# Kernel tuning notes

Hardware: AMD Instinct MI355X
Metric: run time of the kernel (lower is better)

The kernel has to match this reference:

```python
import jax, jax.numpy as jnp
import numpy as np

EPS = 1.0
MAX_ITER = 5
THRESH = 0.01
P_EXP = 2


def setup_inputs() -> dict:
    key = jax.random.key(0)
    k1, k2 = jax.random.split(key)
    x = jax.random.normal(k1, (2, 4096, 3), dtype=jnp.float32)
    y = jax.random.normal(k2, (2, 4096, 3), dtype=jnp.float32)
    return {"x": x, "y": y}


def _cost_matrix(x, y, p=P_EXP):
    # |x_i - y_j|^p summed over feature dim -> (B, P1, P2)
    return jnp.sum(jnp.abs(x[:, :, None, :] - y[:, None, :, :]) ** p, axis=-1)


def reference(x, y):
    C = _cost_matrix(x, y)  # (B, P1, P2)
    B, P1, P2 = C.shape
    log_mu = jnp.full((B, P1), jnp.log(1.0 / P1), dtype=C.dtype)
    log_nu = jnp.full((B, P2), jnp.log(1.0 / P2), dtype=C.dtype)

    def M(u, v):
        # (-C_ij + u_i + v_j) / eps
        return (-C + u[:, :, None] + v[:, None, :]) / EPS

    u = jnp.zeros((B, P1), dtype=C.dtype)
    v = jnp.zeros((B, P2), dtype=C.dtype)
    err = jnp.array(jnp.inf, dtype=C.dtype)
    done = jnp.zeros((), dtype=bool)

    # Unrolled fixed-count loop; `done` freezes updates to emulate the
    # data-dependent early break in the original torch code.
    for i in range(MAX_ITER):
        if i % 2 == 0:
            u_new = EPS * (log_mu - jax.nn.logsumexp(M(u, v), axis=-1)) + u
            err_new = jnp.mean(jnp.sum(jnp.abs(u_new - u), axis=-1))
            u = jnp.where(done, u, u_new)
            err = jnp.where(done, err, err_new)
        else:
            v_new = EPS * (log_nu - jax.nn.logsumexp(M(u, v), axis=-2)) + v
            v = jnp.where(done, v, v_new)
        done = done | (err < THRESH)

    pi = jnp.exp(M(u, v))  # transport plan (B, P1, P2)
    approx_corr_1 = jnp.argmax(pi, axis=-1)  # (B, P1)
    approx_corr_2 = jnp.argmax(pi, axis=-2)  # (B, P2)
    # u.shape[0] == v.shape[0] (== B) so torch takes the sum(dim=-2).sum()
    # branch; both branches reduce to a full sum.
    distance = jnp.sum(pi * C)
    return distance, approx_corr_1, approx_corr_2
```

## Files before the change

kernel.cpp:

```cpp
#include <hip/hip_runtime.h>
#include <math.h>

#define P 4096
#define NB 2
#define NROWS (NB * P)
#define THREADS 512
#define NWAVE (THREADS / 64)
#define R 8
#define NCHUNK (P / THREADS)
#define NBLK (NROWS / R)
#define LOG_INV_P (-8.317766166719343f)
#define INV_P (0.000244140625f)
#define ERR_T (0.02f)

#define WS_U   0
#define WS_V   NROWS
#define WS_ERR (2 * NROWS)
#define WS_SOA 16640


__global__ void prep_kernel(const float* __restrict__ x, const float* __restrict__ y,
                            float* __restrict__ ws, float* __restrict__ out) {
    const int idx = blockIdx.x * blockDim.x + threadIdx.x;
    float* __restrict__ soa = ws + WS_SOA;
    if (idx < NROWS) {
        soa[0 * NROWS + idx] = x[idx * 3 + 0];
        soa[1 * NROWS + idx] = x[idx * 3 + 1];
        soa[2 * NROWS + idx] = x[idx * 3 + 2];
        ws[WS_V + idx] = 0.0f;
    } else {
        const int k = idx - NROWS;
        soa[3 * NROWS + k] = y[k * 3 + 0];
        soa[4 * NROWS + k] = y[k * 3 + 1];
        soa[5 * NROWS + k] = y[k * 3 + 2];
    }
    if (idx < 4) ws[WS_ERR + idx] = 0.0f;
    if (idx == 4) out[0] = 0.0f;
}

template <int WITH_ERR, int ZERO_W>
__global__ __launch_bounds__(THREADS, 4) void lse_single(
    const float* __restrict__ rs0, const float* __restrict__ rs1,
    const float* __restrict__ rs2,
    const float* __restrict__ cs0, const float* __restrict__ cs1,
    const float* __restrict__ cs2,
    const float* __restrict__ w,
    float* __restrict__ pot,
    float* __restrict__ err_acc,
    const float* __restrict__ chk0, const float* __restrict__ chk1)
{
    bool frozen = false;
    if (chk0) frozen = frozen || (*chk0 < ERR_T);
    if (chk1) frozen = frozen || (*chk1 < ERR_T);
    if (frozen) return;

    __shared__ float red[NWAVE * R];

    const int row0 = blockIdx.x * R;
    const int bofs = (row0 >> 12) << 12;
    const int t = threadIdx.x;
    const int wid = t >> 6, lane = t & 63;

    float xr0[R], xr1[R], xr2[R];
#pragma unroll
    for (int r = 0; r < R; r++) {
        xr0[r] = rs0[row0 + r];
        xr1[r] = rs1[row0 + r];
        xr2[r] = rs2[row0 + r];
    }
    float s[R];
#pragma unroll
    for (int r = 0; r < R; r++) s[r] = 0.0f;

#pragma unroll
    for (int k = 0; k < NCHUNK; k++) {
        const int j = bofs + t + k * THREADS;
        const float y0 = cs0[j], y1 = cs1[j], y2 = cs2[j];
        const float wj = ZERO_W ? 0.0f : w[j];
#pragma unroll
        for (int r = 0; r < R; r++) {
            const float d0 = xr0[r] - y0, d1 = xr1[r] - y1, d2 = xr2[r] - y2;
            const float c = d0 * d0 + d1 * d1 + d2 * d2;
            s[r] += __expf(wj - c);
        }
    }
#pragma unroll
    for (int r = 0; r < R; r++) {
        float v2 = s[r];
#pragma unroll
        for (int off = 32; off >= 1; off >>= 1)
            v2 += __shfl_down(v2, off, 64);
        if (lane == 0) red[wid * R + r] = v2;
    }
    __syncthreads();
    if (t < R) {
        float ssum = red[t];
#pragma unroll
        for (int w2 = 1; w2 < NWAVE; w2++) ssum += red[w2 * R + t];
        const float pn = LOG_INV_P - __logf(ssum);
        float d = 0.0f;
        if (WITH_ERR) d = fabsf(pn - (ZERO_W ? 0.0f : pot[row0 + t]));
        pot[row0 + t] = pn;
        if (WITH_ERR) {
#pragma unroll
            for (int off = R / 2; off >= 1; off >>= 1)
                d += __shfl_down(d, off, R);
            if (t == 0) atomicAdd(err_acc, d);
        }
    }
}

__global__ __launch_bounds__(THREADS, 4) void row_final(
    const float* __restrict__ rs0, const float* __restrict__ rs1,
    const float* __restrict__ rs2,
    const float* __restrict__ cs0, const float* __restrict__ cs1,
    const float* __restrict__ cs2,
    const float* __restrict__ v,
    float* __restrict__ u_out,
    float* __restrict__ corr1,
    float* __restrict__ dist)
{
    __shared__ float redS[NWAVE * R];
    __shared__ float redD[NWAVE * R];
    __shared__ float redv[NWAVE * R];
    __shared__ int   redj[NWAVE * R];

    const int row0 = blockIdx.x * R;
    const int bofs = (row0 >> 12) << 12;
    const int t = threadIdx.x;
    const int wid = t >> 6, lane = t & 63;

    float xr0[R], xr1[R], xr2[R];
#pragma unroll
    for (int r = 0; r < R; r++) {
        xr0[r] = rs0[row0 + r];
        xr1[r] = rs1[row0 + r];
        xr2[r] = rs2[row0 + r];
    }
    float S[R], D[R], bv[R];
    int bj[R];
#pragma unroll
    for (int r = 0; r < R; r++) { S[r] = 0.0f; D[r] = 0.0f; bv[r] = -INFINITY; bj[r] = 0; }

#pragma unroll
    for (int k = 0; k < NCHUNK; k++) {
        const int jj = t + k * THREADS;
        const int j = bofs + jj;
        const float y0 = cs0[j], y1 = cs1[j], y2 = cs2[j];
        const float wj = v[j];
#pragma unroll
        for (int r = 0; r < R; r++) {
            const float d0 = xr0[r] - y0, d1 = xr1[r] - y1, d2 = xr2[r] - y2;
            const float c = d0 * d0 + d1 * d1 + d2 * d2;
            const float m = wj - c;
            const float e = __expf(m);
            S[r] += e;
            D[r] += e * c;
            const bool pgt = m > bv[r];
            bj[r] = pgt ? jj : bj[r];
            bv[r] = pgt ? m : bv[r];
        }
    }
#pragma unroll
    for (int r = 0; r < R; r++) {
        float sS = S[r], sD = D[r], v2 = bv[r];
        int j2 = bj[r];
#pragma unroll
        for (int off = 32; off >= 1; off >>= 1) {
            sS += __shfl_down(sS, off, 64);
            sD += __shfl_down(sD, off, 64);
            const float ov = __shfl_down(v2, off, 64);
            const int   oj = __shfl_down(j2, off, 64);
            const bool take = (ov > v2) || (ov == v2 && oj < j2);
            v2 = take ? ov : v2;
            j2 = take ? oj : j2;
        }
        if (lane == 0) {
            redS[wid * R + r] = sS;
            redD[wid * R + r] = sD;
            redv[wid * R + r] = v2;
            redj[wid * R + r] = j2;
        }
    }
    __syncthreads();
    if (t < R) {
        float sS = redS[t], sD = redD[t], v2 = redv[t];
        int j2 = redj[t];
#pragma unroll
        for (int w2 = 1; w2 < NWAVE; w2++) {
            sS += redS[w2 * R + t];
            sD += redD[w2 * R + t];
            const float ov = redv[w2 * R + t];
            const int   oj = redj[w2 * R + t];
            const bool take = (ov > v2) || (ov == v2 && oj < j2);
            v2 = take ? ov : v2;
            j2 = take ? oj : j2;
        }
        u_out[row0 + t] = LOG_INV_P - __logf(sS);
        corr1[row0 + t] = (float)j2;
        float dp = INV_P * sD / sS;
#pragma unroll
        for (int off = R / 2; off >= 1; off >>= 1)
            dp += __shfl_down(dp, off, R);
        if (t == 0) atomicAdd(dist, dp);
    }
}

__global__ __launch_bounds__(THREADS, 4) void col_final(
    const float* __restrict__ rs0, const float* __restrict__ rs1,
    const float* __restrict__ rs2,
    const float* __restrict__ cs0, const float* __restrict__ cs1,
    const float* __restrict__ cs2,
    const float* __restrict__ u,
    float* __restrict__ corr2)
{
    __shared__ float redv[NWAVE * R];
    __shared__ int   redj[NWAVE * R];

    const int row0 = blockIdx.x * R;
    const int bofs = (row0 >> 12) << 12;
    const int t = threadIdx.x;
    const int wid = t >> 6, lane = t & 63;

    float xr0[R], xr1[R], xr2[R];
#pragma unroll
    for (int r = 0; r < R; r++) {
        xr0[r] = rs0[row0 + r];
        xr1[r] = rs1[row0 + r];
        xr2[r] = rs2[row0 + r];
    }
    float bv[R];
    int bj[R];
#pragma unroll
    for (int r = 0; r < R; r++) { bv[r] = -INFINITY; bj[r] = 0; }

#pragma unroll
    for (int k = 0; k < NCHUNK; k++) {
        const int jj = t + k * THREADS;
        const int j = bofs + jj;
        const float y0 = cs0[j], y1 = cs1[j], y2 = cs2[j];
        const float wj = u[j];
#pragma unroll
        for (int r = 0; r < R; r++) {
            const float d0 = xr0[r] - y0, d1 = xr1[r] - y1, d2 = xr2[r] - y2;
            const float c = d0 * d0 + d1 * d1 + d2 * d2;
            const float m = wj - c;
            const bool pgt = m > bv[r];
            bj[r] = pgt ? jj : bj[r];
            bv[r] = pgt ? m : bv[r];
        }
    }
#pragma unroll
    for (int r = 0; r < R; r++) {
        float v2 = bv[r];
        int j2 = bj[r];
#pragma unroll
        for (int off = 32; off >= 1; off >>= 1) {
            const float ov = __shfl_down(v2, off, 64);
            const int   oj = __shfl_down(j2, off, 64);
            const bool take = (ov > v2) || (ov == v2 && oj < j2);
            v2 = take ? ov : v2;
            j2 = take ? oj : j2;
        }
        if (lane == 0) { redv[wid * R + r] = v2; redj[wid * R + r] = j2; }
    }
    __syncthreads();
    if (t < R) {
        float v2 = redv[t];
        int j2 = redj[t];
#pragma unroll
        for (int w2 = 1; w2 < NWAVE; w2++) {
            const float ov = redv[w2 * R + t];
            const int   oj = redj[w2 * R + t];
            const bool take = (ov > v2) || (ov == v2 && oj < j2);
            v2 = take ? ov : v2;
            j2 = take ? oj : j2;
        }
        corr2[row0 + t] = (float)j2;
    }
}

extern "C" void kernel_launch(void* const* d_in, const int* in_sizes, int n_in,
                              void* d_out, int out_size, void* d_ws, size_t ws_size,
                              hipStream_t stream) {
    const float* x = (const float*)d_in[0];
    const float* y = (const float*)d_in[1];
    float* out = (float*)d_out;
    float* ws = (float*)d_ws;

    float* u = ws + WS_U;
    float* v = ws + WS_V;
    float* err = ws + WS_ERR;
    float* xs0 = ws + WS_SOA + 0 * NROWS;
    float* xs1 = ws + WS_SOA + 1 * NROWS;
    float* xs2 = ws + WS_SOA + 2 * NROWS;
    float* ys0 = ws + WS_SOA + 3 * NROWS;
    float* ys1 = ws + WS_SOA + 4 * NROWS;
    float* ys2 = ws + WS_SOA + 5 * NROWS;

    prep_kernel<<<32, 512, 0, stream>>>(x, y, ws, out);

    dim3 grid(NBLK), blk(THREADS);
    lse_single<1, 1><<<grid, blk, 0, stream>>>(xs0, xs1, xs2, ys0, ys1, ys2,
                                               v, u, &err[0], nullptr, nullptr);
    lse_single<0, 0><<<grid, blk, 0, stream>>>(ys0, ys1, ys2, xs0, xs1, xs2,
                                               u, v, nullptr, &err[0], nullptr);
    lse_single<1, 0><<<grid, blk, 0, stream>>>(xs0, xs1, xs2, ys0, ys1, ys2,
                                               v, u, &err[1], &err[0], nullptr);
    lse_single<0, 0><<<grid, blk, 0, stream>>>(ys0, ys1, ys2, xs0, xs1, xs2,
                                               u, v, nullptr, &err[0], &err[1]);
    row_final<<<grid, blk, 0, stream>>>(xs0, xs1, xs2, ys0, ys1, ys2,
                                        v, u, out + 1, out);
    col_final<<<grid, blk, 0, stream>>>(ys0, ys1, ys2, xs0, xs1, xs2,
                                        u, out + 1 + NROWS);
}
```

Measured before the change: 182.2 us.

## Expand squared distance into dot product and work in base-2 log domain

The inputs are prescaled by sqrt(log2 e), and squared norms are precomputed in the prep kernel. The column side stores doubled coordinates, so each cost term becomes three FMAs plus a norm offset fed straight into the hardware v_exp_f32 instruction. All potentials, thresholds and the distance constant are moved into the log2 domain to stay consistent. Column data for all chunks is loaded into registers up front. This cuts per-element ALU work in the compute-bound inner loops, at the cost of some cancellation error from the norm expansion and higher register use.

After: 168.9 us. 7.3% less time.

```diff
diff --git a/kernel.cpp b/kernel.cpp
--- a/kernel.cpp
+++ b/kernel.cpp
@@ -9,30 +9,45 @@
 #define R 8
 #define NCHUNK (P / THREADS)
 #define NBLK (NROWS / R)
-#define LOG_INV_P (-8.317766166719343f)
-#define INV_P (0.000244140625f)
-#define ERR_T (0.02f)
+#define SQRT_LOG2E 1.2011224087864498f
+#define LOG2_INV_P (-12.0f)
+#define ERR_T2 0.028853900817779268f
+#define C_DIST 1.6922538540598323e-4f
 
 #define WS_U   0
 #define WS_V   NROWS
 #define WS_ERR (2 * NROWS)
 #define WS_SOA 16640
 
+
+__device__ __forceinline__ float exp2_hw(float x) {
+    float r;
+    asm("v_exp_f32 %0, %1" : "=v"(r) : "v"(x));
+    return r;
+}
 
 __global__ void prep_kernel(const float* __restrict__ x, const float* __restrict__ y,
                             float* __restrict__ ws, float* __restrict__ out) {
     const int idx = blockIdx.x * blockDim.x + threadIdx.x;
     float* __restrict__ soa = ws + WS_SOA;
     if (idx < NROWS) {
-        soa[0 * NROWS + idx] = x[idx * 3 + 0];
-        soa[1 * NROWS + idx] = x[idx * 3 + 1];
-        soa[2 * NROWS + idx] = x[idx * 3 + 2];
+        const float a0 = x[idx * 3 + 0] * SQRT_LOG2E;
+        const float a1 = x[idx * 3 + 1] * SQRT_LOG2E;
+        const float a2 = x[idx * 3 + 2] * SQRT_LOG2E;
+        soa[0 * NROWS + idx] = a0;
+        soa[1 * NROWS + idx] = a1;
+        soa[2 * NROWS + idx] = a2;
+        soa[3 * NROWS + idx] = a0 * a0 + a1 * a1 + a2 * a2;
         ws[WS_V + idx] = 0.0f;
     } else {
         const int k = idx - NROWS;
-        soa[3 * NROWS + k] = y[k * 3 + 0];
-        soa[4 * NROWS + k] = y[k * 3 + 1];
-        soa[5 * NROWS + k] = y[k * 3 + 2];
+        const float a0 = y[k * 3 + 0] * SQRT_LOG2E;
+        const float a1 = y[k * 3 + 1] * SQRT_LOG2E;
+        const float a2 = y[k * 3 + 2] * SQRT_LOG2E;
+        soa[4 * NROWS + k] = a0 + a0;
+        soa[5 * NROWS + k] = a1 + a1;
+        soa[6 * NROWS + k] = a2 + a2;
+        soa[7 * NROWS + k] = a0 * a0 + a1 * a1 + a2 * a2;
     }
     if (idx < 4) ws[WS_ERR + idx] = 0.0f;
     if (idx == 4) out[0] = 0.0f;
@@ -40,18 +55,18 @@
 
 template <int WITH_ERR, int ZERO_W>
 __global__ __launch_bounds__(THREADS, 4) void lse_single(
-    const float* __restrict__ rs0, const float* __restrict__ rs1,
-    const float* __restrict__ rs2,
-    const float* __restrict__ cs0, const float* __restrict__ cs1,
-    const float* __restrict__ cs2,
-    const float* __restrict__ w,
-    float* __restrict__ pot,
+    const float* __restrict__ rc0, const float* __restrict__ rc1,
+    const float* __restrict__ rc2, const float* __restrict__ rn,
+    const float* __restrict__ cc0, const float* __restrict__ cc1,
+    const float* __restrict__ cc2, const float* __restrict__ cn,
+    const float* __restrict__ w2,
+    float* __restrict__ pot2,
     float* __restrict__ err_acc,
     const float* __restrict__ chk0, const float* __restrict__ chk1)
 {
     bool frozen = false;
-    if (chk0) frozen = frozen || (*chk0 < ERR_T);
-    if (chk1) frozen = frozen || (*chk1 < ERR_T);
+    if (chk0) frozen = frozen || (*chk0 < ERR_T2);
+    if (chk1) frozen = frozen || (*chk1 < ERR_T2);
     if (frozen) return;
 
     __shared__ float red[NWAVE * R];
@@ -60,28 +75,37 @@
     const int bofs = (row0 >> 12) << 12;
     const int t = threadIdx.x;
     const int wid = t >> 6, lane = t & 63;
-
-    float xr0[R], xr1[R], xr2[R];
-#pragma unroll
-    for (int r = 0; r < R; r++) {
-        xr0[r] = rs0[row0 + r];
-        xr1[r] = rs1[row0 + r];
-        xr2[r] = rs2[row0 + r];
-    }
+    const int jbase = bofs + t;
+
+    float r0[R], r1[R], r2[R], rnm[R];
+#pragma unroll
+    for (int r = 0; r < R; r++) {
+        r0[r] = rc0[row0 + r];
+        r1[r] = rc1[row0 + r];
+        r2[r] = rc2[row0 + r];
+        rnm[r] = rn[row0 + r];
+    }
+    float c0[NCHUNK], c1[NCHUNK], c2[NCHUNK], a[NCHUNK];
+#pragma unroll
+    for (int k = 0; k < NCHUNK; k++) {
+        const int j = jbase + k * THREADS;
+        c0[k] = cc0[j];
+        c1[k] = cc1[j];
+        c2[k] = cc2[j];
+        a[k] = (ZERO_W ? 0.0f : w2[j]) - cn[j];
+    }
+
     float s[R];
 #pragma unroll
     for (int r = 0; r < R; r++) s[r] = 0.0f;
 
 #pragma unroll
     for (int k = 0; k < NCHUNK; k++) {
-        const int j = bofs + t + k * THREADS;
-        const float y0 = cs0[j], y1 = cs1[j], y2 = cs2[j];
-        const float wj = ZERO_W ? 0.0f : w[j];
 #pragma unroll
         for (int r = 0; r < R; r++) {
-            const float d0 = xr0[r] - y0, d1 = xr1[r] - y1, d2 = xr2[r] - y2;
-            const float c = d0 * d0 + d1 * d1 + d2 * d2;
-            s[r] += __expf(wj - c);
+            const float b = a[k] - rnm[r];
+            const float m2 = fmaf(c0[k], r0[r], fmaf(c1[k], r1[r], fmaf(c2[k], r2[r], b)));
+            s[r] += exp2_hw(m2);
         }
     }
 #pragma unroll
@@ -96,11 +120,11 @@
     if (t < R) {
         float ssum = red[t];
 #pragma unroll
-        for (int w2 = 1; w2 < NWAVE; w2++) ssum += red[w2 * R + t];
-        const float pn = LOG_INV_P - __logf(ssum);
+        for (int w = 1; w < NWAVE; w++) ssum += red[w * R + t];
+        const float pn = LOG2_INV_P - __log2f(ssum);
         float d = 0.0f;
-        if (WITH_ERR) d = fabsf(pn - (ZERO_W ? 0.0f : pot[row0 + t]));
-        pot[row0 + t] = pn;
+        if (WITH_ERR) d = fabsf(pn - (ZERO_W ? 0.0f : pot2[row0 + t]));
+        pot2[row0 + t] = pn;
         if (WITH_ERR) {
 #pragma unroll
             for (int off = R / 2; off >= 1; off >>= 1)
@@ -111,12 +135,12 @@
 }
 
 __global__ __launch_bounds__(THREADS, 4) void row_final(
-    const float* __restrict__ rs0, const float* __restrict__ rs1,
-    const float* __restrict__ rs2,
-    const float* __restrict__ cs0, const float* __restrict__ cs1,
-    const float* __restrict__ cs2,
-    const float* __restrict__ v,
-    float* __restrict__ u_out,
+    const float* __restrict__ rc0, const float* __restrict__ rc1,
+    const float* __restrict__ rc2, const float* __restrict__ rn,
+    const float* __restrict__ cc0, const float* __restrict__ cc1,
+    const float* __restrict__ cc2, const float* __restrict__ cn,
+    const float* __restrict__ w2,
+    float* __restrict__ u2_out,
     float* __restrict__ corr1,
     float* __restrict__ dist)
 {
@@ -129,14 +153,27 @@
     const int bofs = (row0 >> 12) << 12;
     const int t = threadIdx.x;
     const int wid = t >> 6, lane = t & 63;
-
-    float xr0[R], xr1[R], xr2[R];
-#pragma unroll
-    for (int r = 0; r < R; r++) {
-        xr0[r] = rs0[row0 + r];
-        xr1[r] = rs1[row0 + r];
-        xr2[r] = rs2[row0 + r];
-    }
+    const int jbase = bofs + t;
+
+    float r0[R], r1[R], r2[R], rnm[R];
+#pragma unroll
+    for (int r = 0; r < R; r++) {
+        r0[r] = rc0[row0 + r];
+        r1[r] = rc1[row0 + r];
+        r2[r] = rc2[row0 + r];
+        rnm[r] = rn[row0 + r];
+    }
+    float c0[NCHUNK], c1[NCHUNK], c2[NCHUNK], a[NCHUNK], wv[NCHUNK];
+#pragma unroll
+    for (int k = 0; k < NCHUNK; k++) {
+        const int j = jbase + k * THREADS;
+        c0[k] = cc0[j];
+        c1[k] = cc1[j];
+        c2[k] = cc2[j];
+        wv[k] = w2[j];
+        a[k] = wv[k] - cn[j];
+    }
+
     float S[R], D[R], bv[R];
     int bj[R];
 #pragma unroll
@@ -144,21 +181,16 @@
 
 #pragma unroll
     for (int k = 0; k < NCHUNK; k++) {
-        const int jj = t + k * THREADS;
-        const int j = bofs + jj;
-        const float y0 = cs0[j], y1 = cs1[j], y2 = cs2[j];
-        const float wj = v[j];
 #pragma unroll
         for (int r = 0; r < R; r++) {
-            const float d0 = xr0[r] - y0, d1 = xr1[r] - y1, d2 = xr2[r] - y2;
-            const float c = d0 * d0 + d1 * d1 + d2 * d2;
-            const float m = wj - c;
-            const float e = __expf(m);
+            const float b = a[k] - rnm[r];
+            const float m2 = fmaf(c0[k], r0[r], fmaf(c1[k], r1[r], fmaf(c2[k], r2[r], b)));
+            const float e = exp2_hw(m2);
             S[r] += e;
-            D[r] += e * c;
-            const bool pgt = m > bv[r];
-            bj[r] = pgt ? jj : bj[r];
-            bv[r] = pgt ? m : bv[r];
+            D[r] = fmaf(e, wv[k] - m2, D[r]);
+            const bool pgt = m2 > bv[r];
+            bj[r] = pgt ? (t + k * THREADS) : bj[r];
+            bv[r] = pgt ? m2 : bv[r];
         }
     }
 #pragma unroll
@@ -187,18 +219,18 @@
         float sS = redS[t], sD = redD[t], v2 = redv[t];
         int j2 = redj[t];
 #pragma unroll
-        for (int w2 = 1; w2 < NWAVE; w2++) {
-            sS += redS[w2 * R + t];
-            sD += redD[w2 * R + t];
-            const float ov = redv[w2 * R + t];
-            const int   oj = redj[w2 * R + t];
+        for (int w = 1; w < NWAVE; w++) {
+            sS += redS[w * R + t];
+            sD += redD[w * R + t];
+            const float ov = redv[w * R + t];
+            const int   oj = redj[w * R + t];
             const bool take = (ov > v2) || (ov == v2 && oj < j2);
             v2 = take ? ov : v2;
             j2 = take ? oj : j2;
         }
-        u_out[row0 + t] = LOG_INV_P - __logf(sS);
+        u2_out[row0 + t] = LOG2_INV_P - __log2f(sS);
         corr1[row0 + t] = (float)j2;
-        float dp = INV_P * sD / sS;
+        float dp = C_DIST * sD / sS;
 #pragma unroll
         for (int off = R / 2; off >= 1; off >>= 1)
             dp += __shfl_down(dp, off, R);
@@ -207,11 +239,11 @@
 }
 
 __global__ __launch_bounds__(THREADS, 4) void col_final(
-    const float* __restrict__ rs0, const float* __restrict__ rs1,
-    const float* __restrict__ rs2,
-    const float* __restrict__ cs0, const float* __restrict__ cs1,
-    const float* __restrict__ cs2,
-    const float* __restrict__ u,
+    const float* __restrict__ rc0, const float* __restrict__ rc1,
+    const float* __restrict__ rc2, const float* __restrict__ rn,
+    const float* __restrict__ cc0, const float* __restrict__ cc1,
+    const float* __restrict__ cc2, const float* __restrict__ cn,
+    const float* __restrict__ w2,
     float* __restrict__ corr2)
 {
     __shared__ float redv[NWAVE * R];
@@ -221,14 +253,26 @@
     const int bofs = (row0 >> 12) << 12;
     const int t = threadIdx.x;
     const int wid = t >> 6, lane = t & 63;
-
-    float xr0[R], xr1[R], xr2[R];
-#pragma unroll
-    for (int r = 0; r < R; r++) {
-        xr0[r] = rs0[row0 + r];
-        xr1[r] = rs1[row0 + r];
-        xr2[r] = rs2[row0 + r];
-    }
+    const int jbase = bofs + t;
+
+    float r0[R], r1[R], r2[R], rnm[R];
+#pragma unroll
+    for (int r = 0; r < R; r++) {
+        r0[r] = rc0[row0 + r];
+        r1[r] = rc1[row0 + r];
+        r2[r] = rc2[row0 + r];
+        rnm[r] = rn[row0 + r];
+    }
+    float c0[NCHUNK], c1[NCHUNK], c2[NCHUNK], a[NCHUNK];
+#pragma unroll
+    for (int k = 0; k < NCHUNK; k++) {
+        const int j = jbase + k * THREADS;
+        c0[k] = cc0[j];
+        c1[k] = cc1[j];
+        c2[k] = cc2[j];
+        a[k] = w2[j] - cn[j];
+    }
+
     float bv[R];
     int bj[R];
 #pragma unroll
@@ -236,18 +280,13 @@
 
 #pragma unroll
     for (int k = 0; k < NCHUNK; k++) {
-        const int jj = t + k * THREADS;
-        const int j = bofs + jj;
-        const float y0 = cs0[j], y1 = cs1[j], y2 = cs2[j];
-        const float wj = u[j];
 #pragma unroll
         for (int r = 0; r < R; r++) {
-            const float d0 = xr0[r] - y0, d1 = xr1[r] - y1, d2 = xr2[r] - y2;
-            const float c = d0 * d0 + d1 * d1 + d2 * d2;
-            const float m = wj - c;
-            const bool pgt = m > bv[r];
-            bj[r] = pgt ? jj : bj[r];
-            bv[r] = pgt ? m : bv[r];
+            const float b = a[k] - rnm[r];
+            const float m2 = fmaf(c0[k], r0[r], fmaf(c1[k], r1[r], fmaf(c2[k], r2[r], b)));
+            const bool pgt = m2 > bv[r];
+            bj[r] = pgt ? (t + k * THREADS) : bj[r];
+            bv[r] = pgt ? m2 : bv[r];
         }
     }
 #pragma unroll
@@ -269,9 +308,9 @@
         float v2 = redv[t];
         int j2 = redj[t];
 #pragma unroll
-        for (int w2 = 1; w2 < NWAVE; w2++) {
-            const float ov = redv[w2 * R + t];
-            const int   oj = redj[w2 * R + t];
+        for (int w = 1; w < NWAVE; w++) {
+            const float ov = redv[w * R + t];
+            const int   oj = redj[w * R + t];
             const bool take = (ov > v2) || (ov == v2 && oj < j2);
             v2 = take ? ov : v2;
             j2 = take ? oj : j2;
@@ -288,29 +327,31 @@
     float* out = (float*)d_out;
     float* ws = (float*)d_ws;
 
-    float* u = ws + WS_U;
-    float* v = ws + WS_V;
+    float* u2 = ws + WS_U;
+    float* v2 = ws + WS_V;
     float* err = ws + WS_ERR;
     float* xs0 = ws + WS_SOA + 0 * NROWS;
     float* xs1 = ws + WS_SOA + 1 * NROWS;
     float* xs2 = ws + WS_SOA + 2 * NROWS;
-    float* ys0 = ws + WS_SOA + 3 * NROWS;
-    float* ys1 = ws + WS_SOA + 4 * NROWS;
-    float* ys2 = ws + WS_SOA + 5 * NROWS;
+    float* xn  = ws + WS_SOA + 3 * NROWS;
+    float* ys0 = ws + WS_SOA + 4 * NROWS;
+    float* ys1 = ws + WS_SOA + 5 * NROWS;
+    float* ys2 = ws + WS_SOA + 6 * NROWS;
+    float* yn  = ws + WS_SOA + 7 * NROWS;
 
     prep_kernel<<<32, 512, 0, stream>>>(x, y, ws, out);
 
     dim3 grid(NBLK), blk(THREADS);
-    lse_single<1, 1><<<grid, blk, 0, stream>>>(xs0, xs1, xs2, ys0, ys1, ys2,
-                                               v, u, &err[0], nullptr, nullptr);
-    lse_single<0, 0><<<grid, blk, 0, stream>>>(ys0, ys1, ys2, xs0, xs1, xs2,
-                                               u, v, nullptr, &err[0], nullptr);
-    lse_single<1, 0><<<grid, blk, 0, stream>>>(xs0, xs1, xs2, ys0, ys1, ys2,
-                                               v, u, &err[1], &err[0], nullptr);
-    lse_single<0, 0><<<grid, blk, 0, stream>>>(ys0, ys1, ys2, xs0, xs1, xs2,
-                                               u, v, nullptr, &err[0], &err[1]);
-    row_final<<<grid, blk, 0, stream>>>(xs0, xs1, xs2, ys0, ys1, ys2,
-                                        v, u, out + 1, out);
-    col_final<<<grid, blk, 0, stream>>>(ys0, ys1, ys2, xs0, xs1, xs2,
-                                        u, out + 1 + NROWS);
-}
+    lse_single<1, 1><<<grid, blk, 0, stream>>>(xs0, xs1, xs2, xn, ys0, ys1, ys2, yn,
+                                               v2, u2, &err[0], nullptr, nullptr);
+    lse_single<0, 0><<<grid, blk, 0, stream>>>(ys0, ys1, ys2, yn, xs0, xs1, xs2, xn,
+                                               u2, v2, nullptr, &err[0], nullptr);
+    lse_single<1, 0><<<grid, blk, 0, stream>>>(xs0, xs1, xs2, xn, ys0, ys1, ys2, yn,
+                                               v2, u2, &err[1], &err[0], nullptr);
+    lse_single<0, 0><<<grid, blk, 0, stream>>>(ys0, ys1, ys2, yn, xs0, xs1, xs2, xn,
+                                               u2, v2, nullptr, &err[0], &err[1]);
+    row_final<<<grid, blk, 0, stream>>>(xs0, xs1, xs2, xn, ys0, ys1, ys2, yn,
+                                        v2, u2, out + 1, out);
+    col_final<<<grid, blk, 0, stream>>>(ys0, ys1, ys2, yn, xs0, xs1, xs2, xn,
+                                        u2, out + 1 + NROWS);
+}
```
